# Kernel optimization log

Measured on AMD Instinct MI355X. Metric: run time of the kernel, lower is better.

Reference implementation:

```python
import jax, jax.numpy as jnp
import numpy as np

IN_SIZE = 1024
HIDDEN = 50
OUT_DIM = 8
BATCH = 16384
BN_EPS = 1e-5


def _gf(h, W1, b1, W2, b2):
    # graph_fusion: Linear -> LeakyReLU(0.2) -> Linear -> Tanh
    t = h @ W1 + b1
    t = jnp.where(t > 0, t, 0.2 * t)
    return jnp.tanh(t @ W2 + b2)


def _lrelu(z):
    return jnp.where(z > 0, z, 0.01 * z)  # F.leaky_relu default slope


def _dot(p, q):
    return jnp.sum(p * q, axis=-1)  # batched [B,1,D]@[B,D,1] -> [B]


def setup_inputs() -> dict:
    key = jax.random.key(0)
    ks = jax.random.split(key, 16)
    d, h, o = IN_SIZE, HIDDEN, OUT_DIM
    s = lambda n: 1.0 / np.sqrt(n)
    return {
        "x": jax.random.normal(ks[0], (BATCH, 3, d), jnp.float32),
        "att_W": jax.random.normal(ks[1], (d, 1), jnp.float32) * s(d),
        "att_b": jnp.zeros((1,), jnp.float32),
        "gf_W1": jax.random.normal(ks[2], (2 * d, 64), jnp.float32) * s(2 * d),
        "gf_b1": jnp.zeros((64,), jnp.float32),
        "gf_W2": jax.random.normal(ks[3], (64, d), jnp.float32) * s(64),
        "gf_b2": jnp.zeros((d,), jnp.float32),
        "bn_gamma": jnp.ones((3 * d,), jnp.float32),
        "bn_beta": jnp.zeros((3 * d,), jnp.float32),
        "l1_W": jax.random.normal(ks[4], (3 * d, h), jnp.float32) * s(3 * d),
        "l1_b": jnp.zeros((h,), jnp.float32),
        "l2_W": jax.random.normal(ks[5], (h, h), jnp.float32) * s(h),
        "l2_b": jnp.zeros((h,), jnp.float32),
        "l3_W": jax.random.normal(ks[6], (h, o), jnp.float32) * s(h),
        "l3_b": jnp.zeros((o,), jnp.float32),
    }


def _forward(x, att_W, att_b, gf_W1, gf_b1, gf_W2, gf_b2,
             bn_gamma, bn_beta, l1_W, l1_b, l2_W, l2_b, l3_W, l3_b):
    a1, v1, l1_ = x[:, 0, :], x[:, 1, :], x[:, 2, :]
    gf = lambda p, q: _gf(jnp.concatenate([p, q], axis=1), gf_W1, gf_b1, gf_W2, gf_b2)

    # unimodal attention weights, softmax over the 3 modalities
    att = jnp.tanh(x @ att_W + att_b)[..., 0]          # [B,3]
    w_uni = jax.nn.softmax(att, axis=1)                # [B,3]
    sa, sv, sl = w_uni[:, 0], w_uni[:, 1], w_uni[:, 2]
    unimodal = (sa[:, None] * a1 + sv[:, None] * v1 + sl[:, None] * l1_) / 3.0

    a = jax.nn.softmax(a1, axis=1)
    v = jax.nn.softmax(v1, axis=1)
    l = jax.nn.softmax(l1_, axis=1)
    sav = (sa + sv) / (_dot(a, v) + 0.5)
    sal = (sa + sl) / (_dot(a, l) + 0.5)
    svl = (sl + sv) / (_dot(v, l) + 0.5)
    w_bi = jax.nn.softmax(jnp.stack([sav, sal, svl], axis=1), axis=1)  # [B,3]

    a_v = _lrelu(w_bi[:, 0:1] * gf(a1, v1))
    a_l = _lrelu(w_bi[:, 1:2] * gf(a1, l1_))
    v_l = _lrelu(w_bi[:, 2:3] * gf(v1, l1_))
    bimodal = (a_v + a_l + v_l) / 3.0

    a_v2 = jax.nn.softmax(a_v, axis=1)
    a_l2 = jax.nn.softmax(a_l, axis=1)
    v_l2 = jax.nn.softmax(v_l, axis=1)
    savvl = (sav + svl) / (_dot(a_v2, v_l2) + 0.5)
    saavl = (sav + sal) / (_dot(a_v2, a_l2) + 0.5)
    savll = (sal + svl) / (_dot(a_l2, v_l2) + 0.5)
    savl = (sav + sl) / (_dot(a_v2, l) + 0.5)
    salv = (sal + sv) / (_dot(a_l2, v) + 0.5)
    svla = (sa + svl) / (_dot(v_l2, a) + 0.5)
    w_tri = jax.nn.softmax(
        jnp.stack([savvl, saavl, savll, savl, salv, svla], axis=1), axis=1)  # [B,6]

    avvl = _lrelu(w_tri[:, 0:1] * gf(a_v, v_l))
    aavl = _lrelu(w_tri[:, 1:2] * gf(a_v, a_l))
    avll = _lrelu(w_tri[:, 2:3] * gf(v_l, a_l))
    avl = _lrelu(w_tri[:, 3:4] * gf(a_v, l1_))
    alv = _lrelu(w_tri[:, 4:5] * gf(a_l, v1))
    vla = _lrelu(w_tri[:, 5:6] * gf(v_l, a1))
    trimodal = (avvl + aavl + avll + avl + alv + vla) / 6.0

    fusion = jnp.concatenate([unimodal, bimodal, trimodal], axis=1)  # [B,3*in]
    # BatchNorm1d in eval mode: running_mean=0, running_var=1
    fusion = fusion * (bn_gamma / jnp.sqrt(1.0 + BN_EPS)) + bn_beta
    y = jnp.tanh(fusion @ l1_W + l1_b)
    y = jnp.tanh(y @ l2_W + l2_b)
    y2 = jax.nn.softmax(y @ l3_W + l3_b, axis=1)
    total_weights = jnp.concatenate([w_uni, w_bi, w_tri], axis=1)  # [B,12]
    return y2, total_weights


def reference(x, att_W, att_b, gf_W1, gf_b1, gf_W2, gf_b2,
              bn_gamma, bn_beta, l1_W, l1_b, l2_W, l2_b, l3_W, l3_b):
    return _forward(x, att_W, att_b, gf_W1, gf_b1, gf_W2, gf_b2,
                    bn_gamma, bn_beta, l1_W, l1_b, l2_W, l2_b, l3_W, l3_b)
```

## Files before the change

kernel.cpp:

```cpp
#include <hip/hip_runtime.h>
#include <math.h>

#define NB 16384
#define DD 1024
#define KF 5120

typedef unsigned short u16;
typedef unsigned int u32;
typedef __attribute__((ext_vector_type(8))) short bf16x8;
typedef __attribute__((ext_vector_type(4))) float f32x4;

__device__ __forceinline__ float bf2f(u16 u){
  return __uint_as_float(((unsigned)u) << 16);
}
__device__ __forceinline__ u16 f2bf(float f){
  unsigned u = __float_as_uint(f);
  return (u16)((u + 0x7fffu + ((u >> 16) & 1u)) >> 16);
}
__device__ __forceinline__ u16 f2bf_tr(float f){
  return (u16)(__float_as_uint(f) >> 16);
}
__device__ __forceinline__ u32 pack2bf(float a, float b){
  return (u32)f2bf(a) | ((u32)f2bf(b) << 16);
}
__device__ __forceinline__ float fast_tanh(float x){
  float e = __expf(2.0f * x);
  return 1.0f - 2.0f * __builtin_amdgcn_rcpf(e + 1.0f);
}
__device__ __forceinline__ float wredsum(float x){
  #pragma unroll
  for(int o = 32; o >= 1; o >>= 1) x += __shfl_xor(x, o);
  return x;
}
__device__ __forceinline__ float wredmax(float x){
  #pragma unroll
  for(int o = 32; o >= 1; o >>= 1) x = fmaxf(x, __shfl_xor(x, o));
  return x;
}
__device__ __forceinline__ void gll16(const void* g, void* l){
  __builtin_amdgcn_global_load_lds(
      (const __attribute__((address_space(1))) u32*)g,
      (__attribute__((address_space(3))) u32*)l, 16, 0, 0);
}

__global__ __launch_bounds__(256) void kpre(
    const float* __restrict__ W1, const float* __restrict__ W2,
    const float* __restrict__ gamma, const float* __restrict__ beta,
    const float* __restrict__ l1W, const float* __restrict__ l1b,
    u16* __restrict__ Wb1, u16* __restrict__ W2T, u16* __restrict__ WpT,
    float* __restrict__ bp, float* __restrict__ y1g)
{
  __shared__ float red[4][64];
  int b = blockIdx.x, tid = threadIdx.x;
  if(b < 512){
    int idx = b*256 + tid;
    int n = idx >> 10, k = idx & 1023;
    float v = (n < 64) ? W1[(size_t)k*64 + n] : W1[(size_t)(1024+k)*64 + (n-64)];
    Wb1[idx] = f2bf(v);
  } else if(b < 768){
    int idx = (b-512)*256 + tid;
    int c = idx >> 6, k = idx & 63;
    W2T[idx] = f2bf(W2[(size_t)k*DD + c]);
  } else if(b < 768 + 1280){
    int idx = (b-768)*256 + tid;
    int j = idx / KF, kk = idx - j*KF;
    const float gsc = 1.0f / sqrtf(1.0f + 1e-5f);
    int korig; float sc;
    if(kk < 1024){ korig = kk; sc = 1.f; }
    else if(kk < 4096){ korig = 1024 + ((kk - 1024) & 1023); sc = 1.0f/3.0f; }
    else { korig = 2048 + (kk - 4096); sc = 1.f; }
    float v = (j < 50) ? l1W[(size_t)korig*50 + j] * gamma[korig] * gsc * sc : 0.f;
    WpT[(size_t)j*KF + kk] = f2bf(v);
  } else if(b < 768 + 1280 + 1024){
    int idx = (b - 2048)*256 + tid;
    ((float4*)y1g)[idx] = make_float4(0.f,0.f,0.f,0.f);
  } else {
    int j = tid & 63, seg = tid >> 6;
    float s = 0.f;
    if(j < 50){
      for(int k = seg*768; k < seg*768 + 768; k++)
        s = fmaf(beta[k], l1W[(size_t)k*50 + j], s);
    }
    red[seg][j] = s;
    __syncthreads();
    if(seg == 0){
      float t = red[0][j] + red[1][j] + red[2][j] + red[3][j];
      bp[j] = (j < 50) ? (l1b[j] + t) : 0.f;
    }
  }
}

__global__ __launch_bounds__(256) void k1_stats(
    const float* __restrict__ x, const float* __restrict__ attW,
    const float* __restrict__ attb, float* __restrict__ stats,
    u16* __restrict__ uniB, u16* __restrict__ xb, float* __restrict__ tw)
{
  int wave = threadIdx.x >> 6, lane = threadIdx.x & 63;
  int r = blockIdx.x * 4 + wave;
  const float2* xr  = (const float2*)(x + (size_t)r * 3 * DD);
  const float2* aw2 = (const float2*)attW;
  float2 a[8], v[8], l[8];
  float dA=0.f,dV=0.f,dL=0.f, mA=-1e30f,mV=-1e30f,mL=-1e30f;
  #pragma unroll
  for(int i = 0; i < 8; i++){
    int k2 = lane + i*64;
    a[i] = xr[k2]; v[i] = xr[512+k2]; l[i] = xr[1024+k2];
    float2 w = aw2[k2];
    dA = fmaf(a[i].x, w.x, fmaf(a[i].y, w.y, dA));
    dV = fmaf(v[i].x, w.x, fmaf(v[i].y, w.y, dV));
    dL = fmaf(l[i].x, w.x, fmaf(l[i].y, w.y, dL));
    mA = fmaxf(mA, fmaxf(a[i].x, a[i].y));
    mV = fmaxf(mV, fmaxf(v[i].x, v[i].y));
    mL = fmaxf(mL, fmaxf(l[i].x, l[i].y));
  }
  dA = wredsum(dA); dV = wredsum(dV); dL = wredsum(dL);
  mA = wredmax(mA); mV = wredmax(mV); mL = wredmax(mL);

  u32* xbw = (u32*)(xb + (size_t)3*r*DD);
  #pragma unroll
  for(int i = 0; i < 8; i++){
    int k2 = lane + i*64;
    xbw[k2]      = pack2bf(a[i].x, a[i].y);
    xbw[512+k2]  = pack2bf(v[i].x, v[i].y);
    xbw[1024+k2] = pack2bf(l[i].x, l[i].y);
  }

  float Sa=0.f,Sv=0.f,Sl=0.f,Eav=0.f,Eal=0.f,Evl=0.f;
  #pragma unroll
  for(int i = 0; i < 8; i++){
    float eax = __expf(a[i].x-mA), eay = __expf(a[i].y-mA);
    float evx = __expf(v[i].x-mV), evy = __expf(v[i].y-mV);
    float elx = __expf(l[i].x-mL), ely = __expf(l[i].y-mL);
    Sa += eax+eay; Sv += evx+evy; Sl += elx+ely;
    Eav += eax*evx + eay*evy; Eal += eax*elx + eay*ely; Evl += evx*elx + evy*ely;
  }
  Sa = wredsum(Sa); Sv = wredsum(Sv); Sl = wredsum(Sl);
  Eav = wredsum(Eav); Eal = wredsum(Eal); Evl = wredsum(Evl);

  float ab = attb[0];
  float ta = fast_tanh(dA + ab), tv = fast_tanh(dV + ab), tl = fast_tanh(dL + ab);
  float mm = fmaxf(ta, fmaxf(tv, tl));
  float e0 = __expf(ta-mm), e1 = __expf(tv-mm), e2 = __expf(tl-mm);
  float ss = e0 + e1 + e2;
  float sa = e0/ss, sv = e1/ss, sl = e2/ss;
  float dav = Eav/(Sa*Sv), dal = Eal/(Sa*Sl), dvl = Evl/(Sv*Sl);
  float sav = (sa+sv)/(dav+0.5f);
  float sal = (sa+sl)/(dal+0.5f);
  float svl = (sv+sl)/(dvl+0.5f);
  float m2 = fmaxf(sav, fmaxf(sal, svl));
  float f0 = __expf(sav-m2), f1 = __expf(sal-m2), f2 = __expf(svl-m2);
  float s2 = f0 + f1 + f2;
  float wb0 = f0/s2, wb1 = f1/s2, wb2 = f2/s2;

  if(lane == 0){
    float* st = stats + (size_t)r*24;
    st[0]=sa; st[1]=sv; st[2]=sl;
    st[3]=wb0; st[4]=wb1; st[5]=wb2;
    st[6]=sav; st[7]=sal; st[8]=svl;
    st[9]=mA; st[10]=Sa; st[11]=mV; st[12]=Sv; st[13]=mL; st[14]=Sl;
    float* twr = tw + (size_t)r*12;
    twr[0]=sa; twr[1]=sv; twr[2]=sl; twr[3]=wb0; twr[4]=wb1; twr[5]=wb2;
  }
  u32* uniw = (u32*)(uniB + (size_t)r*DD);
  #pragma unroll
  for(int i = 0; i < 8; i++){
    int k2 = lane + i*64;
    float ux = (sa*a[i].x + sv*v[i].x + sl*l[i].x) * (1.0f/3.0f);
    float uy = (sa*a[i].y + sv*v[i].y + sl*l[i].y) * (1.0f/3.0f);
    uniw[k2] = pack2bf(ux, uy);
  }
}

template<int FCAT>
__global__ __launch_bounds__(256) void kg1v3(
    const u16* __restrict__ src, const u16* __restrict__ Wb1,
    float* __restrict__ UV)
{
  __shared__ u16 Asm[2][64*64];
  int tid = threadIdx.x;
  int wv = tid >> 6, lane = tid & 63;
  int fr = lane & 15, kg = lane >> 4;
  int mb = blockIdx.x * 64;

  int r8 = lane >> 3, p = lane & 7;
  int sp = p ^ r8;
  int m0 = mb + (2*wv)*8 + r8;
  int m1 = mb + (2*wv+1)*8 + r8;
  size_t b0, b1;
  if(FCAT){
    int R0 = m0/3, R1 = m1/3;
    b0 = (size_t)R0*KF + (size_t)(1 + (m0 - 3*R0))*1024;
    b1 = (size_t)R1*KF + (size_t)(1 + (m1 - 3*R1))*1024;
  } else {
    b0 = (size_t)m0*1024;
    b1 = (size_t)m1*1024;
  }
  const u16* gsrc0 = src + b0 + sp*8;
  const u16* gsrc1 = src + b1 + sp*8;

  f32x4 acc[4][2];
  #pragma unroll
  for(int rf = 0; rf < 4; rf++)
    #pragma unroll
    for(int nf = 0; nf < 2; nf++) acc[rf][nf] = (f32x4){0.f,0.f,0.f,0.f};

  gll16(gsrc0, &Asm[0][(2*wv)*512]);
  gll16(gsrc1, &Asm[0][(2*wv+1)*512]);
  __syncthreads();

  int buf = 0;
  for(int ci = 0; ci < 16; ci++){
    int k0 = ci*64;
    if(ci < 15){
      gll16(gsrc0 + k0 + 64, &Asm[buf^1][(2*wv)*512]);
      gll16(gsrc1 + k0 + 64, &Asm[buf^1][(2*wv+1)*512]);
    }
    #pragma unroll
    for(int ks = 0; ks < 2; ks++){
      bf16x8 a[4];
      #pragma unroll
      for(int rf = 0; rf < 4; rf++){
        int row = rf*16 + fr;
        int slot = (ks*4 + kg) ^ (row & 7);
        a[rf] = *(const bf16x8*)&Asm[buf][row*64 + slot*8];
      }
      #pragma unroll
      for(int nf = 0; nf < 2; nf++){
        int col = wv*32 + nf*16 + fr;
        bf16x8 b = *(const bf16x8*)&Wb1[(size_t)col*1024 + k0 + ks*32 + kg*8];
        #pragma unroll
        for(int rf = 0; rf < 4; rf++)
          acc[rf][nf] = __builtin_amdgcn_mfma_f32_16x16x32_bf16(a[rf], b, acc[rf][nf], 0, 0, 0);
      }
    }
    __syncthreads();
    buf ^= 1;
  }

  #pragma unroll
  for(int rf = 0; rf < 4; rf++)
    #pragma unroll
    for(int nf = 0; nf < 2; nf++)
      #pragma unroll
      for(int q = 0; q < 4; q++)
        UV[(size_t)(mb + rf*16 + kg*4 + q)*128 + wv*32 + nf*16 + fr] = acc[rf][nf][q];
}

template<int P, int SUM>
__global__ __launch_bounds__(256) void kL2v5(
    const float* __restrict__ UVA, const float* __restrict__ UVB,
    const u16* __restrict__ W2T, const u16* __restrict__ WpT,
    const float* __restrict__ b1, const float* __restrict__ b2,
    const float* __restrict__ stats, u16* __restrict__ Fcat,
    float* __restrict__ y1g)
{
  const int NO = SUM ? 1 : 4;
  __shared__ u16 Tsm[P][16][64];
  __shared__ u16 Osm[NO][16][264];
  __shared__ float stw[16][8];
  int tid = threadIdx.x;
  int wv = tid >> 6, lane = tid & 63;
  int fr = lane & 15, kg = lane >> 4;
  int Rb = blockIdx.x * 16;

  const int NG = P*16*8;
  for(int i = tid; i < NG; i += 256){
    int g = i & 7, r = (i >> 3) & 15, p = i >> 7;
    int R = Rb + r;
    int up, vp; const float* VBb;
    if(P == 3){
      up = (p == 2) ? 1 : 0;
      vp = (p == 0) ? 1 : 2;
      VBb = UVA;
    } else {
      up = (0x210200 >> (p*4)) & 15;
      vp = (0x012112 >> (p*4)) & 15;
      VBb = (p < 3) ? UVA : UVB;
    }
    const float* Up = UVA + (size_t)(3*R + up)*128 + g*8;
    const float* Vp = VBb + (size_t)(3*R + vp)*128 + 64 + g*8;
    float4 u0 = *(const float4*)Up, u1 = *(const float4*)(Up+4);
    float4 v0 = *(const float4*)Vp, v1 = *(const float4*)(Vp+4);
    float4 bb0 = *(const float4*)(b1 + g*8), bb1 = *(const float4*)(b1 + g*8 + 4);
    float t[8] = {u0.x+v0.x+bb0.x, u0.y+v0.y+bb0.y, u0.z+v0.z+bb0.z, u0.w+v0.w+bb0.w,
                  u1.x+v1.x+bb1.x, u1.y+v1.y+bb1.y, u1.z+v1.z+bb1.z, u1.w+v1.w+bb1.w};
    bf16x8 o;
    #pragma unroll
    for(int j = 0; j < 8; j++){
      float tv = t[j] > 0.f ? t[j] : 0.2f*t[j];
      o[j] = (short)f2bf_tr(tv);
    }
    *(bf16x8*)&Tsm[p][r][(g ^ (r & 7))*8] = o;
  }
  if(tid < 16*P){
    int r = tid / P, p = tid - r*P;
    stw[r][p] = stats[(size_t)(Rb + r)*24 + (SUM ? 15 : 3) + p];
  }
  __syncthreads();

  f32x4 acc[P][4];
  #pragma unroll
  for(int p = 0; p < P; p++)
    #pragma unroll
    for(int cf = 0; cf < 4; cf++) acc[p][cf] = (f32x4){0.f,0.f,0.f,0.f};

  #pragma unroll
  for(int ks = 0; ks < 2; ks++){
    bf16x8 a[P];
    #pragma unroll
    for(int p = 0; p < P; p++)
      a[p] = *(const bf16x8*)&Tsm[p][fr][(((ks<<2)+kg) ^ (fr & 7))*8];
    #pragma unroll
    for(int cf = 0; cf < 4; cf++){
      bf16x8 b = *(const bf16x8*)&W2T[(size_t)(blockIdx.y*256 + wv*64 + cf*16 + fr)*64
                                      + ks*32 + kg*8];
      #pragma unroll
      for(int p = 0; p < P; p++)
        acc[p][cf] = __builtin_amdgcn_mfma_f32_16x16x32_bf16(a[p], b, acc[p][cf], 0, 0, 0);
    }
  }

  #pragma unroll
  for(int q = 0; q < 4; q++){
    int row = kg*4 + q;
    #pragma unroll
    for(int cf = 0; cf < 4; cf++){
      int cloc = wv*64 + cf*16 + fr;
      float b2c = b2[blockIdx.y*256 + cloc];
      if(SUM){
        float s = 0.f;
        #pragma unroll
        for(int p = 0; p < P; p++){
          float g = stw[row][p] * fast_tanh(acc[p][cf][q] + b2c);
          s += g > 0.f ? g : 0.01f*g;
        }
        Osm[0][row][cloc] = f2bf_tr(s * (1.0f/6.0f));
      } else {
        float sm = 0.f;
        #pragma unroll
        for(int p = 0; p < P; p++){
          float g = stw[row][p] * fast_tanh(acc[p][cf][q] + b2c);
          float val = g > 0.f ? g : 0.01f*g;
          Osm[p][row][cloc] = f2bf(val);
          sm += val;
        }
        Osm[3][row][cloc] = f2bf_tr(sm);
      }
    }
  }
  __syncthreads();

  if(!SUM){
    int orow = tid >> 4, oc16 = (tid & 15) * 16;
    #pragma unroll
    for(int p = 0; p < 3; p++){
      bf16x8 o0 = *(const bf16x8*)&Osm[p][orow][oc16];
      bf16x8 o1 = *(const bf16x8*)&Osm[p][orow][oc16 + 8];
      size_t off = (size_t)(Rb + orow)*KF + (size_t)(1+p)*1024 + blockIdx.y*256 + oc16;
      *(bf16x8*)&Fcat[off]     = o0;
      *(bf16x8*)&Fcat[off + 8] = o1;
    }
  }

  {
    size_t kbase = (SUM ? 4096 : 1024) + (size_t)blockIdx.y*256;
    const u16* bptr = WpT + (size_t)(wv*16 + fr)*KF + kbase + kg*8;
    f32x4 accy = (f32x4){0.f,0.f,0.f,0.f};
    #pragma unroll
    for(int kq = 0; kq < 4; kq++)
      #pragma unroll
      for(int ks = 0; ks < 2; ks++){
        bf16x8 a = *(const bf16x8*)&Osm[NO-1][fr][kq*64 + ks*32 + kg*8];
        bf16x8 b = *(const bf16x8*)(bptr + kq*64 + ks*32);
        accy = __builtin_amdgcn_mfma_f32_16x16x32_bf16(a, b, accy, 0, 0, 0);
      }
    #pragma unroll
    for(int q = 0; q < 4; q++)
      atomicAdd(&y1g[(size_t)(Rb + kg*4 + q)*64 + wv*16 + fr], accy[q]);
  }
}

__global__ __launch_bounds__(256) void k3s_v2(
    const u16* __restrict__ Fcat, const u16* __restrict__ xb,
    float* __restrict__ stats, float* __restrict__ tw)
{
  int wave = threadIdx.x >> 6, lane = threadIdx.x & 63;
  int r = blockIdx.x * 4 + wave;
  const u32* pv = (const u32*)(Fcat + (size_t)r*KF + 1024);
  const u32* xv = (const u32*)(xb + (size_t)3*r*DD);

  float* st = stats + (size_t)r*24;
  float sa=st[0], sv=st[1], sl=st[2];
  float sav=st[6], sal=st[7], svl=st[8];
  float mA=st[9], Sa=st[10], mV=st[11], Sv=st[12], mL=st[13], Sl=st[14];

  float Savv=0.f,Sall=0.f,Svll=0.f,E1=0.f,E2=0.f,E3=0.f,E4=0.f,E5=0.f,E6=0.f;
  #pragma unroll
  for(int i = 0; i < 8; i++){
    int k2 = lane + i*64;
    u32 wa = pv[k2], wb = pv[512+k2], wc = pv[1024+k2];
    u32 xa = xv[k2], xvv = xv[512+k2], xl = xv[1024+k2];
    float eavx = __expf(bf2f((u16)wa)),      eavy = __expf(bf2f((u16)(wa>>16)));
    float ealx = __expf(bf2f((u16)wb)),      ealy = __expf(bf2f((u16)(wb>>16)));
    float evlx = __expf(bf2f((u16)wc)),      evly = __expf(bf2f((u16)(wc>>16)));
    float eax  = __expf(bf2f((u16)xa)-mA),   eay  = __expf(bf2f((u16)(xa>>16))-mA);
    float evx  = __expf(bf2f((u16)xvv)-mV),  evy  = __expf(bf2f((u16)(xvv>>16))-mV);
    float elx  = __expf(bf2f((u16)xl)-mL),   ely  = __expf(bf2f((u16)(xl>>16))-mL);
    Savv += eavx+eavy; Sall += ealx+ealy; Svll += evlx+evly;
    E1 += eavx*evlx + eavy*evly; E2 += eavx*ealx + eavy*ealy; E3 += ealx*evlx + ealy*evly;
    E4 += eavx*elx + eavy*ely;   E5 += ealx*evx + ealy*evy;   E6 += evlx*eax + evly*eay;
  }
  Savv = wredsum(Savv); Sall = wredsum(Sall); Svll = wredsum(Svll);
  E1 = wredsum(E1); E2 = wredsum(E2); E3 = wredsum(E3);
  E4 = wredsum(E4); E5 = wredsum(E5); E6 = wredsum(E6);

  float d1 = E1/(Savv*Svll), d2 = E2/(Savv*Sall), d3 = E3/(Sall*Svll);
  float d4 = E4/(Savv*Sl),   d5 = E5/(Sall*Sv),   d6 = E6/(Svll*Sa);
  float t0 = (sav+svl)/(d1+0.5f);
  float t1 = (sav+sal)/(d2+0.5f);
  float t2 = (sal+svl)/(d3+0.5f);
  float t3 = (sav+sl)/(d4+0.5f);
  float t4 = (sal+sv)/(d5+0.5f);
  float t5 = (sa+svl)/(d6+0.5f);
  float mx = fmaxf(fmaxf(fmaxf(t0,t1),fmaxf(t2,t3)),fmaxf(t4,t5));
  float g0=__expf(t0-mx),g1=__expf(t1-mx),g2=__expf(t2-mx);
  float g3=__expf(t3-mx),g4=__expf(t4-mx),g5=__expf(t5-mx);
  float gs = g0+g1+g2+g3+g4+g5;
  if(lane == 0){
    float wt[6] = {g0/gs,g1/gs,g2/gs,g3/gs,g4/gs,g5/gs};
    float* twr = tw + (size_t)r*12;
    #pragma unroll
    for(int p = 0; p < 6; p++){ st[15+p] = wt[p]; twr[6+p] = wt[p]; }
  }
}

__global__ __launch_bounds__(256) void k6v5(
    const u16* __restrict__ uniB, const u16* __restrict__ WpT,
    const float* __restrict__ y1g, const float* __restrict__ bp,
    const float* __restrict__ l2W, const float* __restrict__ l2b,
    const float* __restrict__ l3W, const float* __restrict__ l3b,
    float* __restrict__ y2out)
{
  __shared__ __align__(16) char smem[37952];
  u16*  Asm = (u16*)smem;
  float* W2s = (float*)(smem + 16384);
  float* W3s = (float*)(smem + 16384 + 12800);
  float* Ys  = (float*)smem;
  float* Ys2 = (float*)(smem + 16384 + 12800 + 1600);

  int tid = threadIdx.x;
  int wv = tid >> 6, lane = tid & 63;
  int fr = lane & 15, kg = lane >> 4;
  int rb = blockIdx.x * 32;

  for(int t = tid; t < 3200; t += 256){
    int c = t & 63;
    W2s[t] = (c < 50) ? l2W[(t >> 6)*50 + c] : 0.f;
  }
  for(int t = tid; t < 400; t += 256) W3s[t] = l3W[t];

  int r8 = lane >> 3, pp = lane & 7;
  int sp = pp ^ r8;
  const u16* gsrc = uniB + (size_t)(rb + wv*8 + r8)*DD + sp*8;
  const u16* bptr = WpT  + (size_t)(wv*16 + fr)*KF + kg*8;

  f32x4 acc[2];
  acc[0] = (f32x4){0.f,0.f,0.f,0.f};
  acc[1] = (f32x4){0.f,0.f,0.f,0.f};

  gll16(gsrc,      &Asm[wv*1024]);
  gll16(gsrc + 64, &Asm[wv*1024 + 512]);
  __syncthreads();

  int buf = 0;
  for(int ci = 0; ci < 8; ci++){
    int k0 = ci*128;
    if(ci < 7){
      gll16(gsrc + k0 + 128, &Asm[(buf^1)*4096 + wv*1024]);
      gll16(gsrc + k0 + 192, &Asm[(buf^1)*4096 + wv*1024 + 512]);
    }
    #pragma unroll
    for(int kh = 0; kh < 2; kh++){
      #pragma unroll
      for(int ks = 0; ks < 2; ks++){
        bf16x8 b = *(const bf16x8*)(bptr + k0 + kh*64 + ks*32);
        #pragma unroll
        for(int rf = 0; rf < 2; rf++){
          int row = rf*16 + fr;
          int slot = ((ks<<2) + kg) ^ (row & 7);
          bf16x8 a = *(const bf16x8*)&Asm[buf*4096 + (row>>3)*1024 + kh*512
                                          + (row & 7)*64 + slot*8];
          acc[rf] = __builtin_amdgcn_mfma_f32_16x16x32_bf16(a, b, acc[rf], 0, 0, 0);
        }
      }
    }
    __syncthreads();
    buf ^= 1;
  }

  {
    int col = wv*16 + fr;
    float bpc = bp[col];
    #pragma unroll
    for(int rf = 0; rf < 2; rf++)
      #pragma unroll
      for(int q = 0; q < 4; q++){
        int row = rf*16 + kg*4 + q;
        if(col < 50){
          float z = acc[rf][q] + y1g[(size_t)(rb + row)*64 + col] + bpc;
          Ys[row*56 + col] = fast_tanh(z);
        }
      }
  }
  __syncthreads();

  {
    int r = tid >> 3, cg = (tid & 7) * 7;
    float a2[7] = {0,0,0,0,0,0,0};
    for(int k = 0; k < 50; k++){
      float yv = Ys[r*56 + k];
      #pragma unroll
      for(int c = 0; c < 7; c++) a2[c] = fmaf(yv, W2s[k*64 + cg + c], a2[c]);
    }
    #pragma unroll
    for(int c = 0; c < 7; c++){
      int cc = cg + c;
      if(cc < 50) Ys2[r*56 + cc] = fast_tanh(a2[c] + l2b[cc]);
    }
  }
  __syncthreads();

  {
    int r = tid >> 3, c = tid & 7;
    float z = l3b[c];
    for(int k = 0; k < 50; k++) z = fmaf(Ys2[r*56 + k], W3s[k*8 + c], z);
    float m = z;
    m = fmaxf(m, __shfl_xor(m, 1));
    m = fmaxf(m, __shfl_xor(m, 2));
    m = fmaxf(m, __shfl_xor(m, 4));
    float e = __expf(z - m);
    float s = e;
    s += __shfl_xor(s, 1); s += __shfl_xor(s, 2); s += __shfl_xor(s, 4);
    y2out[(size_t)(rb + r)*8 + c] = e / s;
  }
}

extern "C" void kernel_launch(void* const* d_in, const int* in_sizes, int n_in,
                              void* d_out, int out_size, void* d_ws, size_t ws_size,
                              hipStream_t stream)
{
  (void)in_sizes; (void)n_in; (void)out_size; (void)ws_size;
  const float* x    = (const float*)d_in[0];
  const float* attW = (const float*)d_in[1];
  const float* attb = (const float*)d_in[2];
  const float* gfW1 = (const float*)d_in[3];
  const float* gfb1 = (const float*)d_in[4];
  const float* gfW2 = (const float*)d_in[5];
  const float* gfb2 = (const float*)d_in[6];
  const float* bng  = (const float*)d_in[7];
  const float* bnb  = (const float*)d_in[8];
  const float* l1W  = (const float*)d_in[9];
  const float* l1b  = (const float*)d_in[10];
  const float* l2W  = (const float*)d_in[11];
  const float* l2b  = (const float*)d_in[12];
  const float* l3W  = (const float*)d_in[13];
  const float* l3b  = (const float*)d_in[14];

  float* out = (float*)d_out;
  float* tw  = out + (size_t)NB*8;

  float* ws    = (float*)d_ws;
  float* stats = ws;
  float* UV1   = stats + (size_t)NB*24;
  float* UV2   = UV1 + (size_t)3*NB*128;
  float* bp    = UV2 + (size_t)3*NB*128;
  float* y1g   = bp + 64;
  u16* WpT     = (u16*)(y1g + (size_t)NB*64);
  u16* Wb1     = WpT + (size_t)64*KF;
  u16* W2T     = Wb1 + (size_t)128*1024;
  u16* Fcat    = W2T + (size_t)1024*64;
  u16* xb      = Fcat + (size_t)NB*KF;
  u16* uniB    = xb + (size_t)3*NB*DD;

  kpre<<<dim3(768 + 1280 + 1024 + 1), dim3(256), 0, stream>>>(
      gfW1, gfW2, bng, bnb, l1W, l1b, Wb1, W2T, WpT, bp, y1g);
  k1_stats<<<dim3(NB/4), dim3(256), 0, stream>>>(x, attW, attb, stats, uniB, xb, tw);

  kg1v3<0><<<dim3(3*NB/64), dim3(256), 0, stream>>>(xb, Wb1, UV1);
  kL2v5<3,0><<<dim3(NB/16, 4), dim3(256), 0, stream>>>(UV1, UV1, W2T, WpT,
                                                       gfb1, gfb2, stats, Fcat, y1g);
  k3s_v2<<<dim3(NB/4), dim3(256), 0, stream>>>(Fcat, xb, stats, tw);
  kg1v3<1><<<dim3(3*NB/64), dim3(256), 0, stream>>>(Fcat, Wb1, UV2);
  kL2v5<6,1><<<dim3(NB/16, 4), dim3(256), 0, stream>>>(UV2, UV1, W2T, WpT,
                                                       gfb1, gfb2, stats, Fcat, y1g);
  k6v5<<<dim3(NB/32), dim3(256), 0, stream>>>(uniB, WpT, y1g, bp,
                                              l2W, l2b, l3W, l3b, out);
}
```

Baseline: 392.6 us.

## Fuse bimodal stage with tri-weight stats and second graph-fusion GEMM, drop Fcat

```diff
diff --git a/kernel.cpp b/kernel.cpp
--- a/kernel.cpp
+++ b/kernel.cpp
@@ -48,7 +48,7 @@
     const float* __restrict__ gamma, const float* __restrict__ beta,
     const float* __restrict__ l1W, const float* __restrict__ l1b,
     u16* __restrict__ Wb1, u16* __restrict__ W2T, u16* __restrict__ WpT,
-    float* __restrict__ bp, float* __restrict__ y1g)
+    float* __restrict__ bp)
 {
   __shared__ float red[4][64];
   int b = blockIdx.x, tid = threadIdx.x;
@@ -61,7 +61,7 @@
     int idx = (b-512)*256 + tid;
     int c = idx >> 6, k = idx & 63;
     W2T[idx] = f2bf(W2[(size_t)k*DD + c]);
-  } else if(b < 768 + 1280){
+  } else if(b < 2048){
     int idx = (b-768)*256 + tid;
     int j = idx / KF, kk = idx - j*KF;
     const float gsc = 1.0f / sqrtf(1.0f + 1e-5f);
@@ -71,9 +71,6 @@
     else { korig = 2048 + (kk - 4096); sc = 1.f; }
     float v = (j < 50) ? l1W[(size_t)korig*50 + j] * gamma[korig] * gsc * sc : 0.f;
     WpT[(size_t)j*KF + kk] = f2bf(v);
-  } else if(b < 768 + 1280 + 1024){
-    int idx = (b - 2048)*256 + tid;
-    ((float4*)y1g)[idx] = make_float4(0.f,0.f,0.f,0.f);
   } else {
     int j = tid & 63, seg = tid >> 6;
     float s = 0.f;
@@ -171,7 +168,6 @@
   }
 }
 
-template<int FCAT>
 __global__ __launch_bounds__(256) void kg1v3(
     const u16* __restrict__ src, const u16* __restrict__ Wb1,
     float* __restrict__ UV)
@@ -186,17 +182,8 @@
   int sp = p ^ r8;
   int m0 = mb + (2*wv)*8 + r8;
   int m1 = mb + (2*wv+1)*8 + r8;
-  size_t b0, b1;
-  if(FCAT){
-    int R0 = m0/3, R1 = m1/3;
-    b0 = (size_t)R0*KF + (size_t)(1 + (m0 - 3*R0))*1024;
-    b1 = (size_t)R1*KF + (size_t)(1 + (m1 - 3*R1))*1024;
-  } else {
-    b0 = (size_t)m0*1024;
-    b1 = (size_t)m1*1024;
-  }
-  const u16* gsrc0 = src + b0 + sp*8;
-  const u16* gsrc1 = src + b1 + sp*8;
+  const u16* gsrc0 = src + (size_t)m0*1024 + sp*8;
+  const u16* gsrc1 = src + (size_t)m1*1024 + sp*8;
 
   f32x4 acc[4][2];
   #pragma unroll
@@ -246,39 +233,32 @@
         UV[(size_t)(mb + rf*16 + kg*4 + q)*128 + wv*32 + nf*16 + fr] = acc[rf][nf][q];
 }
 
-template<int P, int SUM>
-__global__ __launch_bounds__(256) void kL2v5(
-    const float* __restrict__ UVA, const float* __restrict__ UVB,
-    const u16* __restrict__ W2T, const u16* __restrict__ WpT,
-    const float* __restrict__ b1, const float* __restrict__ b2,
-    const float* __restrict__ stats, u16* __restrict__ Fcat,
-    float* __restrict__ y1g)
+__global__ __launch_bounds__(256) void kBI(
+    const float* __restrict__ UV1, const u16* __restrict__ xb,
+    const u16* __restrict__ W2T, const u16* __restrict__ Wb1,
+    const u16* __restrict__ WpT, const float* __restrict__ b1,
+    const float* __restrict__ b2, float* __restrict__ stats,
+    float* __restrict__ tw, float* __restrict__ UV2, float* __restrict__ y1g)
 {
-  const int NO = SUM ? 1 : 4;
-  __shared__ u16 Tsm[P][16][64];
-  __shared__ u16 Osm[NO][16][264];
-  __shared__ float stw[16][8];
+  __shared__ u16 Tsm[3][16][64];
+  __shared__ u16 Osm[4][16][264];
+  __shared__ float stro[16][15];
   int tid = threadIdx.x;
   int wv = tid >> 6, lane = tid & 63;
   int fr = lane & 15, kg = lane >> 4;
   int Rb = blockIdx.x * 16;
 
-  const int NG = P*16*8;
-  for(int i = tid; i < NG; i += 256){
+  if(tid < 240){
+    int r = tid / 15, c = tid - r*15;
+    stro[r][c] = stats[(size_t)(Rb + r)*24 + c];
+  }
+  for(int i = tid; i < 384; i += 256){
     int g = i & 7, r = (i >> 3) & 15, p = i >> 7;
     int R = Rb + r;
-    int up, vp; const float* VBb;
-    if(P == 3){
-      up = (p == 2) ? 1 : 0;
-      vp = (p == 0) ? 1 : 2;
-      VBb = UVA;
-    } else {
-      up = (0x210200 >> (p*4)) & 15;
-      vp = (0x012112 >> (p*4)) & 15;
-      VBb = (p < 3) ? UVA : UVB;
-    }
-    const float* Up = UVA + (size_t)(3*R + up)*128 + g*8;
-    const float* Vp = VBb + (size_t)(3*R + vp)*128 + 64 + g*8;
+    int up = (p == 2) ? 1 : 0;
+    int vp = (p == 0) ? 1 : 2;
+    const float* Up = UV1 + (size_t)(3*R + up)*128 + g*8;
+    const float* Vp = UV1 + (size_t)(3*R + vp)*128 + 64 + g*8;
     float4 u0 = *(const float4*)Up, u1 = *(const float4*)(Up+4);
     float4 v0 = *(const float4*)Vp, v1 = *(const float4*)(Vp+4);
     float4 bb0 = *(const float4*)(b1 + g*8), bb1 = *(const float4*)(b1 + g*8 + 4);
@@ -292,54 +272,52 @@
     }
     *(bf16x8*)&Tsm[p][r][(g ^ (r & 7))*8] = o;
   }
-  if(tid < 16*P){
-    int r = tid / P, p = tid - r*P;
-    stw[r][p] = stats[(size_t)(Rb + r)*24 + (SUM ? 15 : 3) + p];
-  }
   __syncthreads();
 
-  f32x4 acc[P][4];
-  #pragma unroll
-  for(int p = 0; p < P; p++)
-    #pragma unroll
-    for(int cf = 0; cf < 4; cf++) acc[p][cf] = (f32x4){0.f,0.f,0.f,0.f};
-
-  #pragma unroll
-  for(int ks = 0; ks < 2; ks++){
-    bf16x8 a[P];
-    #pragma unroll
-    for(int p = 0; p < P; p++)
-      a[p] = *(const bf16x8*)&Tsm[p][fr][(((ks<<2)+kg) ^ (fr & 7))*8];
-    #pragma unroll
-    for(int cf = 0; cf < 4; cf++){
-      bf16x8 b = *(const bf16x8*)&W2T[(size_t)(blockIdx.y*256 + wv*64 + cf*16 + fr)*64
-                                      + ks*32 + kg*8];
-      #pragma unroll
-      for(int p = 0; p < P; p++)
-        acc[p][cf] = __builtin_amdgcn_mfma_f32_16x16x32_bf16(a[p], b, acc[p][cf], 0, 0, 0);
-    }
-  }
-
-  #pragma unroll
-  for(int q = 0; q < 4; q++){
-    int row = kg*4 + q;
-    #pragma unroll
-    for(int cf = 0; cf < 4; cf++){
-      int cloc = wv*64 + cf*16 + fr;
-      float b2c = b2[blockIdx.y*256 + cloc];
-      if(SUM){
-        float s = 0.f;
+  f32x4 acc_uv[3][2];
+  #pragma unroll
+  for(int p = 0; p < 3; p++){ acc_uv[p][0] = (f32x4){0,0,0,0}; acc_uv[p][1] = (f32x4){0,0,0,0}; }
+  f32x4 accy = (f32x4){0,0,0,0};
+  int srow = tid >> 4, sc0 = (tid & 15) * 16;
+  float SP[9] = {0,0,0,0,0,0,0,0,0};
+  float mAr = stro[srow][9],  Sar = stro[srow][10];
+  float mVr = stro[srow][11], Svr = stro[srow][12];
+  float mLr = stro[srow][13], Slr = stro[srow][14];
+  size_t xbase = (size_t)3*(Rb + srow)*DD;
+
+  for(int cg = 0; cg < 4; cg++){
+    f32x4 acc[3][4];
+    #pragma unroll
+    for(int p = 0; p < 3; p++)
+      #pragma unroll
+      for(int cf = 0; cf < 4; cf++) acc[p][cf] = (f32x4){0,0,0,0};
+    #pragma unroll
+    for(int ks = 0; ks < 2; ks++){
+      bf16x8 a[3];
+      #pragma unroll
+      for(int p = 0; p < 3; p++)
+        a[p] = *(const bf16x8*)&Tsm[p][fr][(((ks<<2)+kg) ^ (fr & 7))*8];
+      #pragma unroll
+      for(int cf = 0; cf < 4; cf++){
+        bf16x8 b = *(const bf16x8*)&W2T[(size_t)(cg*256 + wv*64 + cf*16 + fr)*64
+                                        + ks*32 + kg*8];
         #pragma unroll
-        for(int p = 0; p < P; p++){
-          float g = stw[row][p] * fast_tanh(acc[p][cf][q] + b2c);
-          s += g > 0.f ? g : 0.01f*g;
-        }
-        Osm[0][row][cloc] = f2bf_tr(s * (1.0f/6.0f));
-      } else {
+        for(int p = 0; p < 3; p++)
+          acc[p][cf] = __builtin_amdgcn_mfma_f32_16x16x32_bf16(a[p], b, acc[p][cf], 0, 0, 0);
+      }
+    }
+    __syncthreads();
+    #pragma unroll
+    for(int q = 0; q < 4; q++){
+      int row = kg*4 + q;
+      #pragma unroll
+      for(int cf = 0; cf < 4; cf++){
+        int cloc = wv*64 + cf*16 + fr;
+        float b2c = b2[cg*256 + cloc];
         float sm = 0.f;
         #pragma unroll
-        for(int p = 0; p < P; p++){
-          float g = stw[row][p] * fast_tanh(acc[p][cf][q] + b2c);
+        for(int p = 0; p < 3; p++){
+          float g = stro[row][3+p] * fast_tanh(acc[p][cf][q] + b2c);
           float val = g > 0.f ? g : 0.01f*g;
           Osm[p][row][cloc] = f2bf(val);
           sm += val;
@@ -347,90 +325,196 @@
         Osm[3][row][cloc] = f2bf_tr(sm);
       }
     }
+    __syncthreads();
+
+    {
+      const u32* xa1 = (const u32*)(xb + xbase + cg*256 + sc0);
+      const u32* xv1 = (const u32*)(xb + xbase + DD + cg*256 + sc0);
+      const u32* xl1 = (const u32*)(xb + xbase + 2*DD + cg*256 + sc0);
+      #pragma unroll
+      for(int j = 0; j < 8; j++){
+        u32 oav = *(const u32*)&Osm[0][srow][sc0 + 2*j];
+        u32 oal = *(const u32*)&Osm[1][srow][sc0 + 2*j];
+        u32 ovl = *(const u32*)&Osm[2][srow][sc0 + 2*j];
+        u32 wa = xa1[j], wvv = xv1[j], wl = xl1[j];
+        float eavx = __expf(bf2f((u16)oav)), eavy = __expf(bf2f((u16)(oav>>16)));
+        float ealx = __expf(bf2f((u16)oal)), ealy = __expf(bf2f((u16)(oal>>16)));
+        float evlx = __expf(bf2f((u16)ovl)), evly = __expf(bf2f((u16)(ovl>>16)));
+        float eax = __expf(bf2f((u16)wa)-mAr),  eay = __expf(bf2f((u16)(wa>>16))-mAr);
+        float evx = __expf(bf2f((u16)wvv)-mVr), evy = __expf(bf2f((u16)(wvv>>16))-mVr);
+        float elx = __expf(bf2f((u16)wl)-mLr),  ely = __expf(bf2f((u16)(wl>>16))-mLr);
+        SP[0] += eavx+eavy; SP[1] += ealx+ealy; SP[2] += evlx+evly;
+        SP[3] += eavx*evlx + eavy*evly;
+        SP[4] += eavx*ealx + eavy*ealy;
+        SP[5] += ealx*evlx + ealy*evly;
+        SP[6] += eavx*elx + eavy*ely;
+        SP[7] += ealx*evx + ealy*evy;
+        SP[8] += evlx*eax + evly*eay;
+      }
+    }
+    #pragma unroll
+    for(int ks8 = 0; ks8 < 8; ks8++){
+      bf16x8 a[3];
+      #pragma unroll
+      for(int p = 0; p < 3; p++)
+        a[p] = *(const bf16x8*)&Osm[p][fr][ks8*32 + kg*8];
+      #pragma unroll
+      for(int nf = 0; nf < 2; nf++){
+        int n = wv*32 + nf*16 + fr;
+        bf16x8 b = *(const bf16x8*)&Wb1[(size_t)n*1024 + cg*256 + ks8*32 + kg*8];
+        #pragma unroll
+        for(int p = 0; p < 3; p++)
+          acc_uv[p][nf] = __builtin_amdgcn_mfma_f32_16x16x32_bf16(a[p], b, acc_uv[p][nf], 0, 0, 0);
+      }
+    }
+    #pragma unroll
+    for(int kq = 0; kq < 4; kq++)
+      #pragma unroll
+      for(int ks = 0; ks < 2; ks++){
+        bf16x8 a = *(const bf16x8*)&Osm[3][fr][kq*64 + ks*32 + kg*8];
+        bf16x8 b = *(const bf16x8*)&WpT[(size_t)(wv*16 + fr)*KF + 1024 + cg*256
+                                        + kq*64 + ks*32 + kg*8];
+        accy = __builtin_amdgcn_mfma_f32_16x16x32_bf16(a, b, accy, 0, 0, 0);
+      }
+  }
+
+  #pragma unroll
+  for(int p = 0; p < 3; p++)
+    #pragma unroll
+    for(int nf = 0; nf < 2; nf++)
+      #pragma unroll
+      for(int q = 0; q < 4; q++)
+        UV2[(size_t)(3*(Rb + kg*4 + q) + p)*128 + wv*32 + nf*16 + fr] = acc_uv[p][nf][q];
+  #pragma unroll
+  for(int q = 0; q < 4; q++)
+    y1g[(size_t)(Rb + kg*4 + q)*64 + wv*16 + fr] = accy[q];
+
+  #pragma unroll
+  for(int s = 0; s < 9; s++){
+    SP[s] += __shfl_xor(SP[s], 1);
+    SP[s] += __shfl_xor(SP[s], 2);
+    SP[s] += __shfl_xor(SP[s], 4);
+    SP[s] += __shfl_xor(SP[s], 8);
+  }
+  if((tid & 15) == 0){
+    int r = srow;
+    float sa=stro[r][0], sv=stro[r][1], sl=stro[r][2];
+    float sav=stro[r][6], sal=stro[r][7], svl=stro[r][8];
+    float d1 = SP[3]/(SP[0]*SP[2]), d2 = SP[4]/(SP[0]*SP[1]), d3 = SP[5]/(SP[1]*SP[2]);
+    float d4 = SP[6]/(SP[0]*Slr),   d5 = SP[7]/(SP[1]*Svr),   d6 = SP[8]/(SP[2]*Sar);
+    float t0 = (sav+svl)/(d1+0.5f);
+    float t1 = (sav+sal)/(d2+0.5f);
+    float t2 = (sal+svl)/(d3+0.5f);
+    float t3 = (sav+sl)/(d4+0.5f);
+    float t4 = (sal+sv)/(d5+0.5f);
+    float t5 = (sa+svl)/(d6+0.5f);
+    float mx = fmaxf(fmaxf(fmaxf(t0,t1),fmaxf(t2,t3)),fmaxf(t4,t5));
+    float g0=__expf(t0-mx),g1=__expf(t1-mx),g2=__expf(t2-mx);
+    float g3=__expf(t3-mx),g4=__expf(t4-mx),g5=__expf(t5-mx);
+    float gs = g0+g1+g2+g3+g4+g5;
+    float wt[6] = {g0/gs,g1/gs,g2/gs,g3/gs,g4/gs,g5/gs};
+    float* st = stats + (size_t)(Rb + r)*24;
+    float* twr = tw + (size_t)(Rb + r)*12;
+    #pragma unroll
+    for(int p = 0; p < 6; p++){ st[15+p] = wt[p]; twr[6+p] = wt[p]; }
+  }
+}
+
+__global__ __launch_bounds__(256) void kTRI(
+    const float* __restrict__ UV2, const float* __restrict__ UV1,
+    const u16* __restrict__ W2T, const u16* __restrict__ WpT,
+    const float* __restrict__ b1, const float* __restrict__ b2,
+    const float* __restrict__ stats, float* __restrict__ y1g)
+{
+  __shared__ u16 Tsm[6][16][64];
+  __shared__ u16 Osm[16][264];
+  __shared__ float stw[16][6];
+  int tid = threadIdx.x;
+  int wv = tid >> 6, lane = tid & 63;
+  int fr = lane & 15, kg = lane >> 4;
+  int Rb = blockIdx.x * 16;
+
+  if(tid < 96){
+    int r = tid / 6, p = tid - r*6;
+    stw[r][p] = stats[(size_t)(Rb + r)*24 + 15 + p];
+  }
+  for(int i = tid; i < 768; i += 256){
+    int g = i & 7, r = (i >> 3) & 15, p = i >> 7;
+    int R = Rb + r;
+    int up = (0x210200 >> (p*4)) & 15;
+    int vp = (0x012112 >> (p*4)) & 15;
+    const float* VB = (p < 3) ? UV2 : UV1;
+    const float* Up = UV2 + (size_t)(3*R + up)*128 + g*8;
+    const float* Vp = VB  + (size_t)(3*R + vp)*128 + 64 + g*8;
+    float4 u0 = *(const float4*)Up, u1 = *(const float4*)(Up+4);
+    float4 v0 = *(const float4*)Vp, v1 = *(const float4*)(Vp+4);
+    float4 bb0 = *(const float4*)(b1 + g*8), bb1 = *(const float4*)(b1 + g*8 + 4);
+    float t[8] = {u0.x+v0.x+bb0.x, u0.y+v0.y+bb0.y, u0.z+v0.z+bb0.z, u0.w+v0.w+bb0.w,
+                  u1.x+v1.x+bb1.x, u1.y+v1.y+bb1.y, u1.z+v1.z+bb1.z, u1.w+v1.w+bb1.w};
+    bf16x8 o;
+    #pragma unroll
+    for(int j = 0; j < 8; j++){
+      float tv = t[j] > 0.f ? t[j] : 0.2f*t[j];
+      o[j] = (short)f2bf_tr(tv);
+    }
+    *(bf16x8*)&Tsm[p][r][(g ^ (r & 7))*8] = o;
   }
   __syncthreads();
 
-  if(!SUM){
-    int orow = tid >> 4, oc16 = (tid & 15) * 16;
-    #pragma unroll
-    for(int p = 0; p < 3; p++){
-      bf16x8 o0 = *(const bf16x8*)&Osm[p][orow][oc16];
-      bf16x8 o1 = *(const bf16x8*)&Osm[p][orow][oc16 + 8];
-      size_t off = (size_t)(Rb + orow)*KF + (size_t)(1+p)*1024 + blockIdx.y*256 + oc16;
-      *(bf16x8*)&Fcat[off]     = o0;
-      *(bf16x8*)&Fcat[off + 8] = o1;
-    }
-  }
-
-  {
-    size_t kbase = (SUM ? 4096 : 1024) + (size_t)blockIdx.y*256;
-    const u16* bptr = WpT + (size_t)(wv*16 + fr)*KF + kbase + kg*8;
-    f32x4 accy = (f32x4){0.f,0.f,0.f,0.f};
+  f32x4 accy = (f32x4){0,0,0,0};
+  for(int cg = 0; cg < 4; cg++){
+    f32x4 acc[6][4];
+    #pragma unroll
+    for(int p = 0; p < 6; p++)
+      #pragma unroll
+      for(int cf = 0; cf < 4; cf++) acc[p][cf] = (f32x4){0,0,0,0};
+    #pragma unroll
+    for(int ks = 0; ks < 2; ks++){
+      bf16x8 a[6];
+      #pragma unroll
+      for(int p = 0; p < 6; p++)
+        a[p] = *(const bf16x8*)&Tsm[p][fr][(((ks<<2)+kg) ^ (fr & 7))*8];
+      #pragma unroll
+      for(int cf = 0; cf < 4; cf++){
+        bf16x8 b = *(const bf16x8*)&W2T[(size_t)(cg*256 + wv*64 + cf*16 + fr)*64
+                                        + ks*32 + kg*8];
+        #pragma unroll
+        for(int p = 0; p < 6; p++)
+          acc[p][cf] = __builtin_amdgcn_mfma_f32_16x16x32_bf16(a[p], b, acc[p][cf], 0, 0, 0);
+      }
+    }
+    __syncthreads();
+    #pragma unroll
+    for(int q = 0; q < 4; q++){
+      int row = kg*4 + q;
+      #pragma unroll
+      for(int cf = 0; cf < 4; cf++){
+        int cloc = wv*64 + cf*16 + fr;
+        float b2c = b2[cg*256 + cloc];
+        float s = 0.f;
+        #pragma unroll
+        for(int p = 0; p < 6; p++){
+          float g = stw[row][p] * fast_tanh(acc[p][cf][q] + b2c);
+          s += g > 0.f ? g : 0.01f*g;
+        }
+        Osm[row][cloc] = f2bf_tr(s * (1.0f/6.0f));
+      }
+    }
+    __syncthreads();
     #pragma unroll
     for(int kq = 0; kq < 4; kq++)
       #pragma unroll
       for(int ks = 0; ks < 2; ks++){
-        bf16x8 a = *(const bf16x8*)&Osm[NO-1][fr][kq*64 + ks*32 + kg*8];
-        bf16x8 b = *(const bf16x8*)(bptr + kq*64 + ks*32);
+        bf16x8 a = *(const bf16x8*)&Osm[fr][kq*64 + ks*32 + kg*8];
+        bf16x8 b = *(const bf16x8*)&WpT[(size_t)(wv*16 + fr)*KF + 4096 + cg*256
+                                        + kq*64 + ks*32 + kg*8];
         accy = __builtin_amdgcn_mfma_f32_16x16x32_bf16(a, b, accy, 0, 0, 0);
       }
-    #pragma unroll
-    for(int q = 0; q < 4; q++)
-      atomicAdd(&y1g[(size_t)(Rb + kg*4 + q)*64 + wv*16 + fr], accy[q]);
-  }
-}
-
-__global__ __launch_bounds__(256) void k3s_v2(
-    const u16* __restrict__ Fcat, const u16* __restrict__ xb,
-    float* __restrict__ stats, float* __restrict__ tw)
-{
-  int wave = threadIdx.x >> 6, lane = threadIdx.x & 63;
-  int r = blockIdx.x * 4 + wave;
-  const u32* pv = (const u32*)(Fcat + (size_t)r*KF + 1024);
-  const u32* xv = (const u32*)(xb + (size_t)3*r*DD);
-
-  float* st = stats + (size_t)r*24;
-  float sa=st[0], sv=st[1], sl=st[2];
-  float sav=st[6], sal=st[7], svl=st[8];
-  float mA=st[9], Sa=st[10], mV=st[11], Sv=st[12], mL=st[13], Sl=st[14];
-
-  float Savv=0.f,Sall=0.f,Svll=0.f,E1=0.f,E2=0.f,E3=0.f,E4=0.f,E5=0.f,E6=0.f;
-  #pragma unroll
-  for(int i = 0; i < 8; i++){
-    int k2 = lane + i*64;
-    u32 wa = pv[k2], wb = pv[512+k2], wc = pv[1024+k2];
-    u32 xa = xv[k2], xvv = xv[512+k2], xl = xv[1024+k2];
-    float eavx = __expf(bf2f((u16)wa)),      eavy = __expf(bf2f((u16)(wa>>16)));
-    float ealx = __expf(bf2f((u16)wb)),      ealy = __expf(bf2f((u16)(wb>>16)));
-    float evlx = __expf(bf2f((u16)wc)),      evly = __expf(bf2f((u16)(wc>>16)));
-    float eax  = __expf(bf2f((u16)xa)-mA),   eay  = __expf(bf2f((u16)(xa>>16))-mA);
-    float evx  = __expf(bf2f((u16)xvv)-mV),  evy  = __expf(bf2f((u16)(xvv>>16))-mV);
-    float elx  = __expf(bf2f((u16)xl)-mL),   ely  = __expf(bf2f((u16)(xl>>16))-mL);
-    Savv += eavx+eavy; Sall += ealx+ealy; Svll += evlx+evly;
-    E1 += eavx*evlx + eavy*evly; E2 += eavx*ealx + eavy*ealy; E3 += ealx*evlx + ealy*evly;
-    E4 += eavx*elx + eavy*ely;   E5 += ealx*evx + ealy*evy;   E6 += evlx*eax + evly*eay;
-  }
-  Savv = wredsum(Savv); Sall = wredsum(Sall); Svll = wredsum(Svll);
-  E1 = wredsum(E1); E2 = wredsum(E2); E3 = wredsum(E3);
-  E4 = wredsum(E4); E5 = wredsum(E5); E6 = wredsum(E6);
-
-  float d1 = E1/(Savv*Svll), d2 = E2/(Savv*Sall), d3 = E3/(Sall*Svll);
-  float d4 = E4/(Savv*Sl),   d5 = E5/(Sall*Sv),   d6 = E6/(Svll*Sa);
-  float t0 = (sav+svl)/(d1+0.5f);
-  float t1 = (sav+sal)/(d2+0.5f);
-  float t2 = (sal+svl)/(d3+0.5f);
-  float t3 = (sav+sl)/(d4+0.5f);
-  float t4 = (sal+sv)/(d5+0.5f);
-  float t5 = (sa+svl)/(d6+0.5f);
-  float mx = fmaxf(fmaxf(fmaxf(t0,t1),fmaxf(t2,t3)),fmaxf(t4,t5));
-  float g0=__expf(t0-mx),g1=__expf(t1-mx),g2=__expf(t2-mx);
-  float g3=__expf(t3-mx),g4=__expf(t4-mx),g5=__expf(t5-mx);
-  float gs = g0+g1+g2+g3+g4+g5;
-  if(lane == 0){
-    float wt[6] = {g0/gs,g1/gs,g2/gs,g3/gs,g4/gs,g5/gs};
-    float* twr = tw + (size_t)r*12;
-    #pragma unroll
-    for(int p = 0; p < 6; p++){ st[15+p] = wt[p]; twr[6+p] = wt[p]; }
+  }
+  #pragma unroll
+  for(int q = 0; q < 4; q++){
+    size_t idx = (size_t)(Rb + kg*4 + q)*64 + wv*16 + fr;
+    y1g[idx] += accy[q];
   }
 }
 
@@ -578,21 +662,17 @@
   u16* WpT     = (u16*)(y1g + (size_t)NB*64);
   u16* Wb1     = WpT + (size_t)64*KF;
   u16* W2T     = Wb1 + (size_t)128*1024;
-  u16* Fcat    = W2T + (size_t)1024*64;
-  u16* xb      = Fcat + (size_t)NB*KF;
+  u16* xb      = W2T + (size_t)1024*64;
   u16* uniB    = xb + (size_t)3*NB*DD;
 
-  kpre<<<dim3(768 + 1280 + 1024 + 1), dim3(256), 0, stream>>>(
-      gfW1, gfW2, bng, bnb, l1W, l1b, Wb1, W2T, WpT, bp, y1g);
+  kpre<<<dim3(2049), dim3(256), 0, stream>>>(gfW1, gfW2, bng, bnb, l1W, l1b,
+                                             Wb1, W2T, WpT, bp);
   k1_stats<<<dim3(NB/4), dim3(256), 0, stream>>>(x, attW, attb, stats, uniB, xb, tw);
-
-  kg1v3<0><<<dim3(3*NB/64), dim3(256), 0, stream>>>(xb, Wb1, UV1);
-  kL2v5<3,0><<<dim3(NB/16, 4), dim3(256), 0, stream>>>(UV1, UV1, W2T, WpT,
-                                                       gfb1, gfb2, stats, Fcat, y1g);
-  k3s_v2<<<dim3(NB/4), dim3(256), 0, stream>>>(Fcat, xb, stats, tw);
-  kg1v3<1><<<dim3(3*NB/64), dim3(256), 0, stream>>>(Fcat, Wb1, UV2);
-  kL2v5<6,1><<<dim3(NB/16, 4), dim3(256), 0, stream>>>(UV2, UV1, W2T, WpT,
-                                                       gfb1, gfb2, stats, Fcat, y1g);
+  kg1v3<<<dim3(3*NB/64), dim3(256), 0, stream>>>(xb, Wb1, UV1);
+  kBI<<<dim3(NB/16), dim3(256), 0, stream>>>(UV1, xb, W2T, Wb1, WpT,
+                                             gfb1, gfb2, stats, tw, UV2, y1g);
+  kTRI<<<dim3(NB/16), dim3(256), 0, stream>>>(UV2, UV1, W2T, WpT,
+                                              gfb1, gfb2, stats, y1g);
   k6v5<<<dim3(NB/32), dim3(256), 0, stream>>>(uniB, WpT, y1g, bp,
                                               l2W, l2b, l3W, l3b, out);
 }
```

New measurement: 449.9 us. 14.6% more time.
